# Kernel optimization log

Hardware: AMD Instinct MI355X
Metric: run time of the kernel (lower is better)

The kernel has to match this reference:

```python
import jax, jax.numpy as jnp
import numpy as np
import math

EPS = 1e-8


def _cdist(x, y):
    # torch.cdist(p=2) with a grad-safe sqrt (0 grad at zero distance)
    d2 = (jnp.sum(x * x, -1)[:, None] + jnp.sum(y * y, -1)[None, :]
          - 2.0 * x @ y.T)
    d2 = jnp.maximum(d2, 0.0)
    pos = d2 > 0
    return jnp.where(pos, jnp.sqrt(jnp.where(pos, d2, 1.0)), 0.0)


def _metric(proj, dim):
    # [B,D,D] rank-1 + identity, symmetrized, Frobenius-normalized
    m = jnp.einsum('bi,bj->bij', proj, proj) / dim
    m = m + jnp.eye(dim, dtype=proj.dtype)[None]
    m = 0.5 * (m + jnp.swapaxes(m, -2, -1))
    fro = jnp.sqrt(jnp.sum(m * m, axis=(-2, -1), keepdims=True))
    return m / (fro + EPS)


def setup_inputs() -> dict:
    key = jax.random.key(0)
    ks = jax.random.split(key, 4)
    B, D = 4096, 128
    return {
        'query_points': jax.random.normal(ks[0], (B, D), jnp.float32),
        'key_points': jax.random.normal(ks[1], (B, D), jnp.float32),
        'Wq': 0.1 * jax.random.normal(ks[2], (D, D), jnp.float32),
        'bq': jnp.zeros((D,), jnp.float32),
        'Wk': 0.1 * jax.random.normal(ks[3], (D, D), jnp.float32),
        'bk': jnp.zeros((D,), jnp.float32),
    }


def reference(query_points, key_points, Wq, bq, Wk, bk):
    D = Wq.shape[0]
    q = query_points @ Wq.T + bq  # [B,D]
    k = key_points @ Wk.T + bk    # [B,D]
    qm = _metric(q, D)            # [B,D,D]
    km = _metric(k, D)
    q_norm = jnp.sqrt(jnp.einsum('bi,bij,bj->b', q, qm, q))
    k_norm = jnp.sqrt(jnp.einsum('bi,bij,bj->b', k, km, k))
    qn = q / (q_norm[:, None] + EPS)
    kn = k / (k_norm[:, None] + EPS)
    dists = _cdist(qn, kn)                       # [B,B]
    sims = 1.0 / (1.0 + dists)
    temperature = math.sqrt(float(D))
    scores = jax.nn.softmax(sims * temperature, axis=-1)
    score_dists = _cdist(scores, scores)
    input_dists = _cdist(query_points, key_points)
    scale = jnp.mean(input_dists) / (jnp.mean(score_dists) + EPS)
    scores = scores * scale
    scores = scores / (jnp.sum(scores, axis=-1, keepdims=True) + EPS)
    return scores
```

## Files before the change

### kernel.cpp

```cpp
#include <hip/hip_runtime.h>
#include <hip/hip_bf16.h>
#include <math.h>

typedef short short8 __attribute__((ext_vector_type(8)));
typedef float floatx4 __attribute__((ext_vector_type(4)));

#define NB 4096
#define DD 128
static constexpr float EPSF = 1e-8f;
static constexpr float TEMP = 11.313708498984760390f;

static __device__ __forceinline__ short f2bf(float f) {
    __hip_bfloat16 h = __float2bfloat16(f);
    union { __hip_bfloat16 h; short s; } u; u.h = h; return u.s;
}
static __device__ __forceinline__ float bf2f(short s) {
    union { __hip_bfloat16 h; short s; } u; u.s = s;
    return __bfloat162float(u.h);
}

static __device__ __forceinline__ short8 load_cvt8(const float* __restrict__ p) {
    float4 a = *(const float4*)p;
    float4 b = *(const float4*)(p + 4);
    short8 o;
    o[0] = f2bf(a.x); o[1] = f2bf(a.y); o[2] = f2bf(a.z); o[3] = f2bf(a.w);
    o[4] = f2bf(b.x); o[5] = f2bf(b.y); o[6] = f2bf(b.z); o[7] = f2bf(b.w);
    return o;
}

static __device__ __forceinline__ int frag_off(int g, int kidx) {
    return ((((g >> 4) * 4 + (kidx >> 5)) * 4 + ((kidx >> 3) & 3)) * 16
            + (g & 15)) * 8 + (kidx & 7);
}

__global__ __launch_bounds__(256) void proj_kernel(
    const float* __restrict__ qp, const float* __restrict__ kp,
    const float* __restrict__ Wq, const float* __restrict__ bq,
    const float* __restrict__ Wk, const float* __restrict__ bk,
    __hip_bfloat16* __restrict__ qn, __hip_bfloat16* __restrict__ kn,
    float* __restrict__ rq, float* __restrict__ rk)
{
    int t = threadIdx.x;
    int b = blockIdx.x;

    int which = b >> 7;
    int row0 = (b & 127) * 32;
    const float* x    = which ? kp : qp;
    const float* W    = which ? Wk : Wq;
    const float* bias = which ? bk : bq;
    short* outv = which ? (short*)kn : (short*)qn;
    float* outr = which ? rk : rq;

    int lane = t & 63, wid = t >> 6;
    int m = lane & 15, quad = lane >> 4;
    int colb = wid * 32;

    floatx4 acc[2][2];
    #pragma unroll
    for (int i = 0; i < 2; ++i)
        #pragma unroll
        for (int j = 0; j < 2; ++j)
            acc[i][j] = (floatx4){0.f, 0.f, 0.f, 0.f};

    #pragma unroll
    for (int ks = 0; ks < 4; ++ks) {
        int koff = ks * 32 + quad * 8;
        short8 af[2], bfr[2];
        #pragma unroll
        for (int rt = 0; rt < 2; ++rt)
            af[rt] = load_cvt8(x + (row0 + rt*16 + m) * DD + koff);
        #pragma unroll
        for (int ct = 0; ct < 2; ++ct)
            bfr[ct] = load_cvt8(W + (colb + ct*16 + m) * DD + koff);
        #pragma unroll
        for (int rt = 0; rt < 2; ++rt)
            #pragma unroll
            for (int ct = 0; ct < 2; ++ct)
                acc[rt][ct] = __builtin_amdgcn_mfma_f32_16x16x32_bf16(
                    af[rt], bfr[ct], acc[rt][ct], 0, 0, 0);
    }

    __shared__ float buf[4][32];
    __shared__ float nfb[32];

    float bv[2];
    #pragma unroll
    for (int ct = 0; ct < 2; ++ct) bv[ct] = bias[colb + ct*16 + m];

    #pragma unroll
    for (int rt = 0; rt < 2; ++rt) {
        #pragma unroll
        for (int r = 0; r < 4; ++r) {
            float p = 0.0f;
            #pragma unroll
            for (int ct = 0; ct < 2; ++ct) {
                float v = acc[rt][ct][r] + bv[ct];
                acc[rt][ct][r] = v;
                p = fmaf(v, v, p);
            }
            p += __shfl_xor(p, 1); p += __shfl_xor(p, 2);
            p += __shfl_xor(p, 4); p += __shfl_xor(p, 8);
            if (m == 0) buf[wid][rt*16 + quad*4 + r] = p;
        }
    }
    __syncthreads();
    if (t < 32) {
        float s = buf[0][t] + buf[1][t] + buf[2][t] + buf[3][t];
        float fro = sqrtf(s*s*(1.0f/16384.0f) + s*(1.0f/64.0f) + 128.0f);
        float qnorm = sqrtf((s*s*(1.0f/128.0f) + s) / (fro + EPSF));
        nfb[t] = 1.0f / (qnorm + EPSF);
    }
    __syncthreads();

    #pragma unroll
    for (int rt = 0; rt < 2; ++rt) {
        #pragma unroll
        for (int r = 0; r < 4; ++r) {
            int lrow = rt*16 + quad*4 + r;
            int g = row0 + lrow;
            float nf = nfb[lrow];
            float u = 0.0f;
            #pragma unroll
            for (int ct = 0; ct < 2; ++ct) {
                float v = acc[rt][ct][r] * nf;
                short sb = f2bf(v);
                outv[frag_off(g, colb + ct*16 + m)] = sb;
                float vf = bf2f(sb);
                u = fmaf(vf, vf, u);
            }
            u += __shfl_xor(u, 1); u += __shfl_xor(u, 2);
            u += __shfl_xor(u, 4); u += __shfl_xor(u, 8);
            if (m == 0) buf[wid][lrow] = u;
        }
    }
    __syncthreads();
    if (t < 32)
        outr[row0 + t] = buf[0][t] + buf[1][t] + buf[2][t] + buf[3][t];
}

__global__ __launch_bounds__(1024) void score_rows(
    const __hip_bfloat16* __restrict__ qn, const __hip_bfloat16* __restrict__ kn,
    const float* __restrict__ rq, const float* __restrict__ rk,
    float* __restrict__ P)
{
    int lane = threadIdx.x & 63;
    int wid  = threadIdx.x >> 6;
    int m    = lane & 15;
    int quad = lane >> 4;

    int rowblk = blockIdx.x;
    int r0 = rowblk * 16;
    int cs = wid * 256;

    const short* qs  = (const short*)qn;
    const short* kks = (const short*)kn;

    short8 af[4];
    #pragma unroll
    for (int k4 = 0; k4 < 4; ++k4)
        af[k4] = *(const short8*)(qs + ((rowblk*4 + k4)*64 + lane)*8);

    float rqv[4];
    #pragma unroll
    for (int r = 0; r < 4; ++r) rqv[r] = rq[r0 + quad*4 + r];

    floatx4 acc[4][4];
    float rs[4] = {0.f, 0.f, 0.f, 0.f};

    #pragma unroll
    for (int it = 0; it < 4; ++it) {
        #pragma unroll
        for (int ct = 0; ct < 4; ++ct) {
            int colblk = (cs >> 4) + it*4 + ct;
            short8 bfr[4];
            #pragma unroll
            for (int k4 = 0; k4 < 4; ++k4)
                bfr[k4] = *(const short8*)(kks + ((colblk*4 + k4)*64 + lane)*8);
            floatx4 a = (floatx4){0.f, 0.f, 0.f, 0.f};
            #pragma unroll
            for (int k4 = 0; k4 < 4; ++k4)
                a = __builtin_amdgcn_mfma_f32_16x16x32_bf16(af[k4], bfr[k4], a, 0, 0, 0);
            float rkv = rk[colblk*16 + m];
            #pragma unroll
            for (int r = 0; r < 4; ++r) {
                float d2 = fmaf(-2.0f, a[r], rqv[r] + rkv);
                float d  = d2 > 0.0f ? __builtin_amdgcn_sqrtf(d2) : 0.0f;
                float e  = __expf(TEMP * __builtin_amdgcn_rcpf(1.0f + d));
                a[r] = e;
                rs[r] += e;
            }
            acc[it][ct] = a;
        }
    }

    #pragma unroll
    for (int r = 0; r < 4; ++r) {
        rs[r] += __shfl_xor(rs[r], 1); rs[r] += __shfl_xor(rs[r], 2);
        rs[r] += __shfl_xor(rs[r], 4); rs[r] += __shfl_xor(rs[r], 8);
    }

    __shared__ float sums[16][16];
    __shared__ float inv[16];
    if (m == 0) {
        #pragma unroll
        for (int r = 0; r < 4; ++r) sums[wid][quad*4 + r] = rs[r];
    }
    __syncthreads();
    if (threadIdx.x < 16) {
        float s = 0.f;
        #pragma unroll
        for (int w = 0; w < 16; ++w) s += sums[w][threadIdx.x];
        inv[threadIdx.x] = __builtin_amdgcn_rcpf(s + EPSF);
    }
    __syncthreads();

    float invv[4];
    #pragma unroll
    for (int r = 0; r < 4; ++r) invv[r] = inv[quad*4 + r];

    #pragma unroll
    for (int it = 0; it < 4; ++it) {
        #pragma unroll
        for (int ct = 0; ct < 4; ++ct) {
            #pragma unroll
            for (int r = 0; r < 4; ++r) {
                long row = r0 + quad*4 + r;
                P[row * NB + cs + it*64 + ct*16 + m] = acc[it][ct][r] * invv[r];
            }
        }
    }
}

extern "C" void kernel_launch(void* const* d_in, const int* in_sizes, int n_in,
                              void* d_out, int out_size, void* d_ws, size_t ws_size,
                              hipStream_t stream) {
    const float* qp = (const float*)d_in[0];
    const float* kp = (const float*)d_in[1];
    const float* Wq = (const float*)d_in[2];
    const float* bq = (const float*)d_in[3];
    const float* Wk = (const float*)d_in[4];
    const float* bk = (const float*)d_in[5];
    float* P = (float*)d_out;

    char* ws = (char*)d_ws;
    __hip_bfloat16* qn = (__hip_bfloat16*)ws;
    __hip_bfloat16* kn = (__hip_bfloat16*)(ws + (size_t)NB*DD*2);
    float* rq = (float*)(ws + (size_t)NB*DD*4);
    float* rk = (float*)(ws + (size_t)NB*DD*4 + (size_t)NB*4);

    hipLaunchKernelGGL(proj_kernel, dim3(256), dim3(256), 0, stream,
                       qp, kp, Wq, bq, Wk, bk, qn, kn, rq, rk);
    hipLaunchKernelGGL(score_rows, dim3(256), dim3(1024), 0, stream,
                       qn, kn, rq, rk, P);
}
```

Baseline: 117.9 us.

## Transpose MFMA operands so each lane owns a row and stores float4 columns

Swaps the A/B operands of the MFMA so the accumulator is transposed: each lane now holds four consecutive columns of one row instead of four rows of one column. This lets the output be written as 16-byte vector stores (nontemporal) instead of scattered 4-byte stores, and cuts the row-sum reduction from four 4-step shuffles to two shuffles. The rk values become a float4 load while rq becomes a single scalar. The aim is to reduce store-instruction count and improve write coalescing on the 64MB output, which dominates runtime.

```diff
diff --git a/kernel.cpp b/kernel.cpp
--- a/kernel.cpp
+++ b/kernel.cpp
@@ -160,12 +160,10 @@
     for (int k4 = 0; k4 < 4; ++k4)
         af[k4] = *(const short8*)(qs + ((rowblk*4 + k4)*64 + lane)*8);
 
-    float rqv[4];
-    #pragma unroll
-    for (int r = 0; r < 4; ++r) rqv[r] = rq[r0 + quad*4 + r];
+    float rqv = rq[r0 + m];
 
     floatx4 acc[4][4];
-    float rs[4] = {0.f, 0.f, 0.f, 0.f};
+    float rs = 0.f;
 
     #pragma unroll
     for (int it = 0; it < 4; ++it) {
@@ -179,32 +177,26 @@
             floatx4 a = (floatx4){0.f, 0.f, 0.f, 0.f};
             #pragma unroll
             for (int k4 = 0; k4 < 4; ++k4)
-                a = __builtin_amdgcn_mfma_f32_16x16x32_bf16(af[k4], bfr[k4], a, 0, 0, 0);
-            float rkv = rk[colblk*16 + m];
+                a = __builtin_amdgcn_mfma_f32_16x16x32_bf16(bfr[k4], af[k4], a, 0, 0, 0);
+            floatx4 rkv = *(const floatx4*)(rk + colblk*16 + quad*4);
             #pragma unroll
             for (int r = 0; r < 4; ++r) {
-                float d2 = fmaf(-2.0f, a[r], rqv[r] + rkv);
+                float d2 = fmaf(-2.0f, a[r], rqv + rkv[r]);
                 float d  = d2 > 0.0f ? __builtin_amdgcn_sqrtf(d2) : 0.0f;
                 float e  = __expf(TEMP * __builtin_amdgcn_rcpf(1.0f + d));
                 a[r] = e;
-                rs[r] += e;
+                rs += e;
             }
             acc[it][ct] = a;
         }
     }
 
-    #pragma unroll
-    for (int r = 0; r < 4; ++r) {
-        rs[r] += __shfl_xor(rs[r], 1); rs[r] += __shfl_xor(rs[r], 2);
-        rs[r] += __shfl_xor(rs[r], 4); rs[r] += __shfl_xor(rs[r], 8);
-    }
+    rs += __shfl_xor(rs, 16);
+    rs += __shfl_xor(rs, 32);
 
     __shared__ float sums[16][16];
     __shared__ float inv[16];
-    if (m == 0) {
-        #pragma unroll
-        for (int r = 0; r < 4; ++r) sums[wid][quad*4 + r] = rs[r];
-    }
+    if (lane < 16) sums[wid][lane] = rs;
     __syncthreads();
     if (threadIdx.x < 16) {
         float s = 0.f;
@@ -214,19 +206,16 @@
     }
     __syncthreads();
 
-    float invv[4];
-    #pragma unroll
-    for (int r = 0; r < 4; ++r) invv[r] = inv[quad*4 + r];
+    float invv = inv[m];
 
     #pragma unroll
     for (int it = 0; it < 4; ++it) {
         #pragma unroll
         for (int ct = 0; ct < 4; ++ct) {
-            #pragma unroll
-            for (int r = 0; r < 4; ++r) {
-                long row = r0 + quad*4 + r;
-                P[row * NB + cs + it*64 + ct*16 + m] = acc[it][ct][r] * invv[r];
-            }
+            floatx4 o = acc[it][ct] * invv;
+            floatx4* dst = (floatx4*)(P + (size_t)(r0 + m) * NB
+                                        + cs + it*64 + ct*16 + quad*4);
+            __builtin_nontemporal_store(o, dst);
         }
     }
 }
```

Result: slower. 127.3 us (+8.0%).
